# Kernel optimization log

Hardware: AMD Instinct MI355X
Metric: run time of the kernel (lower is better)

Reference implementation:

```python
import jax, jax.numpy as jnp
import numpy as np
import math

HIDDEN = 2048
NUM_HEADS = 32
NUM_KV_HEADS = 8
HEAD_DIM = HIDDEN // NUM_HEADS  # 64
GROUPS = NUM_HEADS // NUM_KV_HEADS  # 4
ROPE_THETA = 10000.0
TOPK_FRAC = 0.5
BSZ, QLEN = 1, 2048


def setup_inputs() -> dict:
    key = jax.random.key(0)
    ks = jax.random.split(key, 6)
    s = 0.02
    return {
        "hidden_states": jax.random.normal(ks[0], (BSZ, QLEN, HIDDEN), jnp.float32),
        "Wq": jax.random.normal(ks[1], (HIDDEN, HIDDEN), jnp.float32) * s,
        "Wk": jax.random.normal(ks[2], (NUM_KV_HEADS * HEAD_DIM, HIDDEN), jnp.float32) * s,
        "Wv": jax.random.normal(ks[3], (NUM_KV_HEADS * HEAD_DIM, HIDDEN), jnp.float32) * s,
        "Wo": jax.random.normal(ks[4], (HIDDEN, HIDDEN), jnp.float32) * s,
        "Wpred": jax.random.normal(ks[5], (NUM_HEADS, HIDDEN), jnp.float32) * s,
        "position_ids": jnp.tile(jnp.arange(QLEN, dtype=jnp.int32), (BSZ, 1)),
    }


def _rotate_half(x):
    h = x.shape[-1] // 2
    return jnp.concatenate([-x[..., h:], x[..., :h]], axis=-1)


def _rope_cos_sin(position_ids, dtype):
    inv_freq = 1.0 / (ROPE_THETA ** (jnp.arange(0, HEAD_DIM, 2, dtype=jnp.float32) / HEAD_DIM))
    freqs = position_ids.astype(jnp.float32)[..., None] * inv_freq  # [b, q, d/2]
    emb = jnp.concatenate([freqs, freqs], axis=-1)                  # [b, q, d]
    return jnp.cos(emb).astype(dtype), jnp.sin(emb).astype(dtype)


def _head_mask(hidden_states, Wpred):
    # predictor logits per token -> top-k heads -> binary mask [b, H, q]
    logits = jnp.einsum('bqh,nh->bqn', hidden_states.astype(jnp.float32), Wpred.astype(jnp.float32))
    k = int(NUM_HEADS * TOPK_FRAC)
    _, idx = jax.lax.top_k(logits, k)                    # [b, q, k]
    mask = jax.nn.one_hot(idx, NUM_HEADS, dtype=hidden_states.dtype).sum(axis=-2)  # [b, q, H]
    return jax.lax.stop_gradient(jnp.swapaxes(mask, 1, 2))  # [b, H, q]


def reference(hidden_states, Wq, Wk, Wv, Wo, Wpred, position_ids):
    b, q_len, _ = hidden_states.shape
    dtype = hidden_states.dtype

    head_mask = _head_mask(hidden_states, Wpred)

    q = (hidden_states @ Wq.T).reshape(b, q_len, NUM_HEADS, HEAD_DIM).transpose(0, 2, 1, 3)
    k = (hidden_states @ Wk.T).reshape(b, q_len, NUM_KV_HEADS, HEAD_DIM).transpose(0, 2, 1, 3)
    v = (hidden_states @ Wv.T).reshape(b, q_len, NUM_KV_HEADS, HEAD_DIM).transpose(0, 2, 1, 3)

    cos, sin = _rope_cos_sin(position_ids, dtype)  # [b, q, d]
    cos, sin = cos[:, None], sin[:, None]          # [b, 1, q, d]
    q = q * cos + _rotate_half(q) * sin
    k = k * cos + _rotate_half(k) * sin

    # repeat_kv (GQA)
    k = jnp.repeat(k, GROUPS, axis=1)  # [b, H, q, d]
    v = jnp.repeat(v, GROUPS, axis=1)

    scores = jnp.einsum('bhqd,bhkd->bhqk', q, k) / math.sqrt(HEAD_DIM)
    causal = jnp.triu(jnp.full((q_len, q_len), -1e9, dtype=scores.dtype), k=1)
    scores = scores + causal
    attn = jax.nn.softmax(scores.astype(jnp.float32), axis=-1).astype(dtype)

    out = jnp.einsum('bhqk,bhkd->bhqd', attn, v)
    out = out * head_mask[..., None]               # gate inactive heads
    out = out.transpose(0, 2, 1, 3).reshape(b, q_len, HIDDEN)
    return out @ Wo.T
```

## Files before the change

### kernel.cpp

```cpp
#include <hip/hip_runtime.h>
#include <hip/hip_bf16.h>

#define HIDDEN 2048
#define NHEADS 32
#define NKV 8
#define HD 64
#define QLEN 2048

typedef short bf16x8 __attribute__((ext_vector_type(8)));
typedef float f32x4 __attribute__((ext_vector_type(4)));
typedef float f32x16 __attribute__((ext_vector_type(16)));

static __device__ __forceinline__ unsigned short f2bf(float f) {
  unsigned int u = __float_as_uint(f);
  u += 0x7fff + ((u >> 16) & 1);
  return (unsigned short)(u >> 16);
}
static __device__ __forceinline__ float bf2f(unsigned short h) {
  return __uint_as_float(((unsigned int)h) << 16);
}
static __device__ __forceinline__ unsigned pack_bf2(float lo, float hi) {
  __hip_bfloat162 h2 = __float22bfloat162_rn(make_float2(lo, hi));
  unsigned u; __builtin_memcpy(&u, &h2, 4); return u;
}

#define GL16(gsrc, ldst) \
  __builtin_amdgcn_global_load_lds((const __attribute__((address_space(1))) unsigned int*)(gsrc), \
                                   (__attribute__((address_space(3))) unsigned int*)(ldst), 16, 0, 0)
#define MFMA32(a, b, c) __builtin_amdgcn_mfma_f32_32x32x16_bf16((a), (b), (c), 0, 0, 0)

__global__ __launch_bounds__(256) void cvt_all_kernel(const float* __restrict__ p0, const float* __restrict__ p1,
                                                      const float* __restrict__ p2, const float* __restrict__ p3,
                                                      const float* __restrict__ p4,
                                                      unsigned short* __restrict__ q0, unsigned short* __restrict__ q1,
                                                      unsigned short* __restrict__ q2, unsigned short* __restrict__ q3,
                                                      unsigned short* __restrict__ q4) {
  const int n0 = 1048576, n1 = 2097152, n2 = 2359296, n3 = 2621440, n4 = 3670016;
  for (int t = blockIdx.x * 256 + threadIdx.x; t < n4; t += gridDim.x * 256) {
    const float4* src; unsigned short* dst; int off;
    if (t < n0)      { src = (const float4*)p0; dst = q0; off = t; }
    else if (t < n1) { src = (const float4*)p1; dst = q1; off = t - n0; }
    else if (t < n2) { src = (const float4*)p2; dst = q2; off = t - n1; }
    else if (t < n3) { src = (const float4*)p3; dst = q3; off = t - n2; }
    else             { src = (const float4*)p4; dst = q4; off = t - n3; }
    float4 v = src[off];
    ushort4 o;
    o.x = f2bf(v.x); o.y = f2bf(v.y); o.z = f2bf(v.z); o.w = f2bf(v.w);
    ((ushort4*)dst)[off] = o;
  }
}

__global__ void rope_table_kernel(const int* __restrict__ pid, float* __restrict__ cost, float* __restrict__ sint) {
  int t = blockIdx.x * blockDim.x + threadIdx.x;
  if (t >= QLEN * 32) return;
  int pos = t >> 5, j = t & 31;
  float p = (float)pid[pos];
  float inv = exp2f(-(float)j * 0.41524101187358740f);
  float f = p * inv;
  cost[t] = cosf(f);
  sint[t] = sinf(f);
}

__global__ __launch_bounds__(256) void wpt_kernel(const float* __restrict__ Wpred, float* __restrict__ WpT) {
  int k = blockIdx.x * 256 + threadIdx.x;
  float v[32];
#pragma unroll
  for (int h = 0; h < 32; ++h) v[h] = Wpred[(size_t)h * HIDDEN + k];
  float4* o = (float4*)(WpT + (size_t)k * 32);
#pragma unroll
  for (int j = 0; j < 8; ++j) o[j] = make_float4(v[4*j], v[4*j+1], v[4*j+2], v[4*j+3]);
}

__global__ __launch_bounds__(256) void headmask_part_kernel(const float* __restrict__ hs,
                                                            const float* __restrict__ WpT,
                                                            double* __restrict__ part) {
  const int tid = threadIdx.x;
  const int ql = tid >> 5, hh = tid & 31;
  const int q = blockIdx.x * 8 + ql;
  const int ks = blockIdx.y;
  const float* hr = hs + (size_t)q * HIDDEN + ks * 512;
  const float* wp = WpT + (size_t)ks * 512 * 32 + hh;
  double a0 = 0.0, a1 = 0.0;
#pragma unroll 4
  for (int k = 0; k < 512; k += 4) {
    float4 hv = *(const float4*)(hr + k);
    float w0 = wp[(k + 0) * 32];
    float w1 = wp[(k + 1) * 32];
    float w2 = wp[(k + 2) * 32];
    float w3 = wp[(k + 3) * 32];
    a0 += (double)hv.x * (double)w0 + (double)hv.y * (double)w1;
    a1 += (double)hv.z * (double)w2 + (double)hv.w * (double)w3;
  }
  part[((size_t)ks * QLEN + q) * 32 + hh] = a0 + a1;
}

__global__ __launch_bounds__(256) void headmask_comb_kernel(const double* __restrict__ part,
                                                            float* __restrict__ mask) {
  __shared__ float lg[8][32];
  const int tid = threadIdx.x;
  const int ql = tid >> 5, hh = tid & 31;
  const int q = blockIdx.x * 8 + ql;
  double s = part[(size_t)q * 32 + hh]
           + part[((size_t)QLEN + q) * 32 + hh]
           + part[((size_t)2 * QLEN + q) * 32 + hh]
           + part[((size_t)3 * QLEN + q) * 32 + hh];
  float mine = (float)s;
  lg[ql][hh] = mine;
  __syncthreads();
  int rank = 0;
#pragma unroll
  for (int j = 0; j < NHEADS; ++j) {
    float oj = lg[ql][j];
    if (oj > mine || (oj == mine && j < hh)) ++rank;
  }
  mask[(size_t)hh * QLEN + q] = (rank < 16) ? 1.0f : 0.0f;
}

__global__ void rope_apply_kernel(unsigned short* __restrict__ X,
                                  const float* __restrict__ cost, const float* __restrict__ sint,
                                  int nh, int rowstride, int total) {
  int t = blockIdx.x * blockDim.x + threadIdx.x;
  if (t >= total) return;
  int j = t & 31;
  int h = (t >> 5) % nh;
  int pos = t / (32 * nh);
  size_t base = (size_t)pos * rowstride + h * HD;
  float x0 = bf2f(X[base + j]);
  float x1 = bf2f(X[base + 32 + j]);
  float c = cost[pos * 32 + j];
  float s = sint[pos * 32 + j];
  X[base + j]      = f2bf(x0 * c - x1 * s);
  X[base + 32 + j] = f2bf(x1 * c + x0 * s);
}

__global__ __launch_bounds__(256) void transpose_kernel(const unsigned short* __restrict__ in,
                                                        unsigned short* __restrict__ out,
                                                        int R, int C, int ldin) {
  __shared__ unsigned short t[64][72];
  int r0 = blockIdx.y * 64, c0 = blockIdx.x * 64;
  int tid = threadIdx.x;
  int rr = tid >> 3;
  int cc = (tid & 7) * 8;
#pragma unroll
  for (int c = 0; c < 2; ++c) {
    int row = rr + c * 32;
    *(bf16x8*)&t[row][cc] = *(const bf16x8*)(in + (size_t)(r0 + row) * ldin + c0 + cc);
  }
  __syncthreads();
#pragma unroll
  for (int c = 0; c < 2; ++c) {
    int oc = rr + c * 32;
    union { unsigned short s[8]; bf16x8 v; } o;
#pragma unroll
    for (int j = 0; j < 8; ++j) o.s[j] = t[cc + j][oc];
    *(bf16x8*)(out + (size_t)(c0 + oc) * R + r0 + cc) = o.v;
  }
}

template<bool OUT_BF16>
__global__ __launch_bounds__(256) void gemm2_kernel(const unsigned short* __restrict__ A,
                                                    const unsigned short* __restrict__ B,
                                                    void* __restrict__ Cout, int N, int K) {
  __shared__ __align__(16) unsigned short As[128 * 32];
  __shared__ __align__(16) unsigned short Bs[128 * 32];
  const int tid = threadIdx.x;
  const int w = tid >> 6, l = tid & 63;
  const int lr = l & 15, lg = l >> 4;
  const int n0 = blockIdx.x * 128, m0 = blockIdx.y * 128;
  const int wm = (w >> 1) * 64, wn = (w & 1) * 64;
  f32x4 acc[4][4] = {};
  const int srow = w * 16 + (l >> 2);
  const int scol = (l & 3) * 8;
  const unsigned short* ap0 = A + (size_t)(m0 + srow) * K + scol;
  const unsigned short* ap1 = ap0 + (size_t)64 * K;
  const unsigned short* bp0 = B + (size_t)(n0 + srow) * K + scol;
  const unsigned short* bp1 = bp0 + (size_t)64 * K;
  unsigned short* asl0 = As + w * 512;
  unsigned short* asl1 = As + 2048 + w * 512;
  unsigned short* bsl0 = Bs + w * 512;
  unsigned short* bsl1 = Bs + 2048 + w * 512;
  for (int k0 = 0; k0 < K; k0 += 32) {
    GL16(ap0 + k0, asl0);
    GL16(ap1 + k0, asl1);
    GL16(bp0 + k0, bsl0);
    GL16(bp1 + k0, bsl1);
    __syncthreads();
    bf16x8 af[4], bfr[4];
#pragma unroll
    for (int m = 0; m < 4; ++m) af[m] = *(const bf16x8*)(As + (wm + m * 16 + lr) * 32 + lg * 8);
#pragma unroll
    for (int n = 0; n < 4; ++n) bfr[n] = *(const bf16x8*)(Bs + (wn + n * 16 + lr) * 32 + lg * 8);
#pragma unroll
    for (int m = 0; m < 4; ++m)
#pragma unroll
      for (int n = 0; n < 4; ++n)
        acc[m][n] = __builtin_amdgcn_mfma_f32_16x16x32_bf16(af[m], bfr[n], acc[m][n], 0, 0, 0);
    __syncthreads();
  }
#pragma unroll
  for (int m = 0; m < 4; ++m) {
    int row = m0 + wm + m * 16 + lg * 4;
#pragma unroll
    for (int n = 0; n < 4; ++n) {
      int col = n0 + wn + n * 16 + lr;
#pragma unroll
      for (int r = 0; r < 4; ++r) {
        if (OUT_BF16)
          ((unsigned short*)Cout)[(size_t)(row + r) * N + col] = f2bf(acc[m][n][r]);
        else
          ((float*)Cout)[(size_t)(row + r) * N + col] = acc[m][n][r];
      }
    }
  }
}

__global__ __launch_bounds__(128) void attn5_kernel(const unsigned short* __restrict__ Q,
                                                    const unsigned short* __restrict__ KV,
                                                    const unsigned short* __restrict__ VT,
                                                    const float* __restrict__ cost,
                                                    const float* __restrict__ sint,
                                                    const float* __restrict__ mask,
                                                    unsigned short* __restrict__ AO) {
  __shared__ __align__(16) unsigned short sm[2][4096];
  const int tid = threadIdx.x;
  const int w = tid >> 6, l = tid & 63;
  const int hi = l >> 5, l31 = l & 31;
  const int h = blockIdx.y, kvh = h >> 2;
  const int qt = 31 - blockIdx.x;
  const int qrow = qt * 64 + w * 32 + l31;
  const int swz = (l & 7) << 4;
  const int hi16 = hi << 4;
  const float DEFER_T = 11.5415603f;

  const int strow = l >> 3;
  const int scol = ((l & 7) ^ strow) * 8;
  const unsigned short* kp0 = KV + (size_t)((0 + w) * 8 + strow) * 1024 + kvh * 64 + scol;
  const unsigned short* kp1 = KV + (size_t)((2 + w) * 8 + strow) * 1024 + kvh * 64 + scol;
  const unsigned short* kp2 = KV + (size_t)((4 + w) * 8 + strow) * 1024 + kvh * 64 + scol;
  const unsigned short* kp3 = KV + (size_t)((6 + w) * 8 + strow) * 1024 + kvh * 64 + scol;

#define STAGE(kt_, b_) do { \
    const size_t kko_ = (size_t)(kt_) * 65536; \
    unsigned short* smb_ = &sm[b_][0]; \
    GL16(kp0 + kko_, smb_ + (0 + w) * 512); \
    GL16(kp1 + kko_, smb_ + (2 + w) * 512); \
    GL16(kp2 + kko_, smb_ + (4 + w) * 512); \
    GL16(kp3 + kko_, smb_ + (6 + w) * 512); \
  } while (0)

  const float QSC = 0.125f * 1.44269504088896340736f;
  const unsigned short* qp = Q + (size_t)qrow * HIDDEN + h * HD + hi * 8;
  bf16x8 qv0 = *(const bf16x8*)qp;
  bf16x8 qv1 = *(const bf16x8*)(qp + 16);
  bf16x8 qv2 = *(const bf16x8*)(qp + 32);
  bf16x8 qv3 = *(const bf16x8*)(qp + 48);
  const float* cbp = cost + qrow * 32 + hi * 8;
  const float* sbp = sint + qrow * 32 + hi * 8;
  f32x4 ca0 = *(const f32x4*)cbp,        ca1 = *(const f32x4*)(cbp + 4);
  f32x4 cB0 = *(const f32x4*)(cbp + 16), cB1 = *(const f32x4*)(cbp + 20);
  f32x4 sa0 = *(const f32x4*)sbp,        sa1 = *(const f32x4*)(sbp + 4);
  f32x4 sB0 = *(const f32x4*)(sbp + 16), sB1 = *(const f32x4*)(sbp + 20);
  bf16x8 qr0, qr1, qr2, qr3;
#pragma unroll
  for (int j = 0; j < 8; ++j) {
    float cosA = j < 4 ? ca0[j] : ca1[j - 4];
    float sinA = j < 4 ? sa0[j] : sa1[j - 4];
    float cosB = j < 4 ? cB0[j] : cB1[j - 4];
    float sinB = j < 4 ? sB0[j] : sB1[j - 4];
    float x0 = bf2f((unsigned short)qv0[j]);
    float x1 = bf2f((unsigned short)qv1[j]);
    float x2 = bf2f((unsigned short)qv2[j]);
    float x3 = bf2f((unsigned short)qv3[j]);
    qr0[j] = (short)f2bf((x0 * cosA - x2 * sinA) * QSC);
    qr1[j] = (short)f2bf((x1 * cosB - x3 * sinB) * QSC);
    qr2[j] = (short)f2bf((x2 * cosA + x0 * sinA) * QSC);
    qr3[j] = (short)f2bf((x3 * cosB + x1 * sinB) * QSC);
  }

  f32x16 O0 = {}, O1 = {};
  float mR = -1e30f, sR = 0.f;
  int cur = 0;
  STAGE(0, 0);
  __syncthreads();

  for (int kt = 0; kt <= qt; ++kt) {
    if (kt < qt) STAGE(kt + 1, cur ^ 1);

    const char* Kc = (const char*)&sm[cur][0];

    f32x16 sA = {}, sB = {};
#define KF(half, dc) (*(const bf16x8*)(Kc + (((half) * 32 + l31) << 7) + ((((dc) * 32 + hi16)) ^ swz)))
    sA = MFMA32(KF(0, 0), qr0, sA);
    sA = MFMA32(KF(0, 1), qr1, sA);
    sA = MFMA32(KF(0, 2), qr2, sA);
    sA = MFMA32(KF(0, 3), qr3, sA);
    sB = MFMA32(KF(1, 0), qr0, sB);
    sB = MFMA32(KF(1, 1), qr1, sB);
    sB = MFMA32(KF(1, 2), qr2, sB);
    sB = MFMA32(KF(1, 3), qr3, sB);
#undef KF

    bf16x8 vf[2][4];
#pragma unroll
    for (int n = 0; n < 2; ++n)
#pragma unroll
      for (int kc = 0; kc < 4; ++kc)
        vf[n][kc] = *(const bf16x8*)(VT + (size_t)(kvh * 64 + n * 32 + l31) * QLEN
                                        + kt * 64 + kc * 16 + hi * 8);

    if (kt == qt) {
      const int wql = w * 32 + l31;
#pragma unroll
      for (int r = 0; r < 16; ++r) {
        int key = (r & 3) + 8 * (r >> 2) + 4 * hi;
        if (key > wql) sA[r] = -1e30f;
        if (32 + key > wql) sB[r] = -1e30f;
      }
    }

#define MAX8(v, o) fmaxf(fmaxf(fmaxf(v[o], v[o+1]), fmaxf(v[o+2], v[o+3])), \
                         fmaxf(fmaxf(v[o+4], v[o+5]), fmaxf(v[o+6], v[o+7])))
    float mx = fmaxf(fmaxf(MAX8(sA, 0), MAX8(sA, 8)), fmaxf(MAX8(sB, 0), MAX8(sB, 8)));
#undef MAX8
    mx = fmaxf(mx, __shfl_xor(mx, 32));
    bool renorm = __any(mx - mR > DEFER_T);
    if (renorm) {
      float mn = fmaxf(mR, mx);
      float sc = exp2f(mR - mn);
      mR = mn;
      sR *= sc;
#pragma unroll
      for (int r = 0; r < 16; ++r) { O0[r] *= sc; O1[r] *= sc; }
    }
#pragma unroll
    for (int r = 0; r < 16; ++r) sA[r] = exp2f(sA[r] - mR);
#pragma unroll
    for (int r = 0; r < 16; ++r) sB[r] = exp2f(sB[r] - mR);
#define SUM8(v, o) (((v[o] + v[o+1]) + (v[o+2] + v[o+3])) + ((v[o+4] + v[o+5]) + (v[o+6] + v[o+7])))
    float rs = (SUM8(sA, 0) + SUM8(sA, 8)) + (SUM8(sB, 0) + SUM8(sB, 8));
#undef SUM8
    rs += __shfl_xor(rs, 32);
    sR += rs;

    bf16x8 pf[4];
#pragma unroll
    for (int kc = 0; kc < 4; ++kc) {
      const int r0 = (kc & 1) * 8;
      float p0, p1, p2, p3, p4, p5, p6, p7;
      if (kc & 2) { p0 = sB[r0+0]; p1 = sB[r0+1]; p2 = sB[r0+2]; p3 = sB[r0+3];
                    p4 = sB[r0+4]; p5 = sB[r0+5]; p6 = sB[r0+6]; p7 = sB[r0+7]; }
      else        { p0 = sA[r0+0]; p1 = sA[r0+1]; p2 = sA[r0+2]; p3 = sA[r0+3];
                    p4 = sA[r0+4]; p5 = sA[r0+5]; p6 = sA[r0+6]; p7 = sA[r0+7]; }
      unsigned a_ = pack_bf2(p0, p1);
      unsigned c_ = pack_bf2(p2, p3);
      unsigned b_ = pack_bf2(p4, p5);
      unsigned d_ = pack_bf2(p6, p7);
      unsigned ax = __shfl_xor(a_, 32), bx2 = __shfl_xor(b_, 32);
      unsigned cx = __shfl_xor(c_, 32), dx = __shfl_xor(d_, 32);
      union { unsigned u[4]; bf16x8 v; } uu;
      uu.u[0] = hi ? bx2 : a_;
      uu.u[1] = hi ? dx : c_;
      uu.u[2] = hi ? b_ : ax;
      uu.u[3] = hi ? d_ : cx;
      pf[kc] = uu.v;
    }

    O0 = MFMA32(vf[0][0], pf[0], O0);
    O1 = MFMA32(vf[1][0], pf[0], O1);
    O0 = MFMA32(vf[0][1], pf[1], O0);
    O1 = MFMA32(vf[1][1], pf[1], O1);
    O0 = MFMA32(vf[0][2], pf[2], O0);
    O1 = MFMA32(vf[1][2], pf[2], O1);
    O0 = MFMA32(vf[0][3], pf[3], O0);
    O1 = MFMA32(vf[1][3], pf[3], O1);

    __syncthreads();
    cur ^= 1;
  }

  float msk = mask[(size_t)h * QLEN + qrow];
  float inv = msk / sR;
  unsigned short* aop = AO + (size_t)qrow * HIDDEN + h * HD;
#pragma unroll
  for (int rp = 0; rp < 8; ++rp) {
    int r = rp * 2;
    int d0 = (r & 3) + 8 * (r >> 2) + 4 * hi;
    *(unsigned*)(aop + d0)      = pack_bf2(O0[r] * inv, O0[r + 1] * inv);
    *(unsigned*)(aop + 32 + d0) = pack_bf2(O1[r] * inv, O1[r + 1] * inv);
  }
#undef STAGE
}

extern "C" void kernel_launch(void* const* d_in, const int* in_sizes, int n_in,
                              void* d_out, int out_size, void* d_ws, size_t ws_size,
                              hipStream_t stream) {
  const float* hs    = (const float*)d_in[0];
  const float* Wq    = (const float*)d_in[1];
  const float* Wk    = (const float*)d_in[2];
  const float* Wv    = (const float*)d_in[3];
  const float* Wo    = (const float*)d_in[4];
  const float* Wpred = (const float*)d_in[5];
  const int*   pid   = (const int*)d_in[6];
  float* out = (float*)d_out;

  unsigned short* hsb = (unsigned short*)d_ws;
  unsigned short* Wqb = hsb + 4194304;
  unsigned short* Wkb = Wqb + 4194304;
  unsigned short* Wvb = Wkb + 1048576;
  unsigned short* Wob = Wvb + 1048576;
  unsigned short* Qb  = Wob + 4194304;
  unsigned short* KVb = Qb  + 4194304;
  unsigned short* AOb = KVb + 2097152;
  float* maskb = (float*)(AOb + 4194304);
  float* cost  = maskb + 65536;
  float* sint  = cost + 65536;
  float* WpT   = sint + 65536;
  double* hmp  = (double*)(WpT + 65536);
  unsigned short* VTb = hsb;

  cvt_all_kernel<<<2048, 256, 0, stream>>>(hs, Wq, Wk, Wv, Wo, hsb, Wqb, Wkb, Wvb, Wob);

  rope_table_kernel<<<256, 256, 0, stream>>>(pid, cost, sint);

  wpt_kernel<<<8, 256, 0, stream>>>(Wpred, WpT);
  headmask_part_kernel<<<dim3(256, 4), 256, 0, stream>>>(hs, WpT, hmp);
  headmask_comb_kernel<<<256, 256, 0, stream>>>(hmp, maskb);

  gemm2_kernel<true><<<dim3(16, 16), 256, 0, stream>>>(hsb, Wqb, Qb, 2048, 2048);
  gemm2_kernel<true><<<dim3(8, 16), 256, 0, stream>>>(hsb, Wkb, KVb, 1024, 2048);

  rope_apply_kernel<<<2048, 256, 0, stream>>>(KVb, cost, sint, NKV, 1024, QLEN * NKV * 32);

  transpose_kernel<<<dim3(8, 32), 256, 0, stream>>>(KVb + 512, VTb, QLEN, 512, 1024);

  attn5_kernel<<<dim3(32, 32), 128, 0, stream>>>(Qb, KVb, VTb, cost, sint, maskb, AOb);

  gemm2_kernel<false><<<dim3(16, 16), 256, 0, stream>>>(AOb, Wob, out, 2048, 2048);
}
```

Baseline: 374.8 us.

## Fuse Q and KV projections into one GEMM; widen attention tile and stage V in LDS

The Q and KV projection GEMMs merge into one launch over a 24-column grid, which relies on Wq, Wk and Wv sitting contiguously in memory as one combined weight. The attention kernel now handles 128 query rows per block with 4 waves, so each K/V tile staged into LDS is shared by twice as many queries. V tiles are also staged into LDS alongside K instead of being read from global memory per wave. Waves whose causal range ends early skip compute but still join the barriers, which adds some idle time and halves the block count.

```diff
diff --git a/kernel.cpp b/kernel.cpp
--- a/kernel.cpp
+++ b/kernel.cpp
@@ -154,6 +154,64 @@
 #pragma unroll
     for (int j = 0; j < 8; ++j) o.s[j] = t[cc + j][oc];
     *(bf16x8*)(out + (size_t)(c0 + oc) * R + r0 + cc) = o.v;
+  }
+}
+
+__global__ __launch_bounds__(256) void gemm_qkv_kernel(const unsigned short* __restrict__ A,
+                                                       const unsigned short* __restrict__ B,
+                                                       unsigned short* __restrict__ Qo,
+                                                       unsigned short* __restrict__ KVo) {
+  const int K = 2048;
+  __shared__ __align__(16) unsigned short As[128 * 32];
+  __shared__ __align__(16) unsigned short Bs[128 * 32];
+  const int tid = threadIdx.x;
+  const int w = tid >> 6, l = tid & 63;
+  const int lr = l & 15, lg = l >> 4;
+  const int n0 = blockIdx.x * 128, m0 = blockIdx.y * 128;
+  const int wm = (w >> 1) * 64, wn = (w & 1) * 64;
+  f32x4 acc[4][4] = {};
+  const int srow = w * 16 + (l >> 2);
+  const int scol = (l & 3) * 8;
+  const unsigned short* ap0 = A + (size_t)(m0 + srow) * K + scol;
+  const unsigned short* ap1 = ap0 + (size_t)64 * K;
+  const unsigned short* bp0 = B + (size_t)(n0 + srow) * K + scol;
+  const unsigned short* bp1 = bp0 + (size_t)64 * K;
+  unsigned short* asl0 = As + w * 512;
+  unsigned short* asl1 = As + 2048 + w * 512;
+  unsigned short* bsl0 = Bs + w * 512;
+  unsigned short* bsl1 = Bs + 2048 + w * 512;
+  for (int k0 = 0; k0 < K; k0 += 32) {
+    GL16(ap0 + k0, asl0);
+    GL16(ap1 + k0, asl1);
+    GL16(bp0 + k0, bsl0);
+    GL16(bp1 + k0, bsl1);
+    __syncthreads();
+    bf16x8 af[4], bfr[4];
+#pragma unroll
+    for (int m = 0; m < 4; ++m) af[m] = *(const bf16x8*)(As + (wm + m * 16 + lr) * 32 + lg * 8);
+#pragma unroll
+    for (int n = 0; n < 4; ++n) bfr[n] = *(const bf16x8*)(Bs + (wn + n * 16 + lr) * 32 + lg * 8);
+#pragma unroll
+    for (int m = 0; m < 4; ++m)
+#pragma unroll
+      for (int n = 0; n < 4; ++n)
+        acc[m][n] = __builtin_amdgcn_mfma_f32_16x16x32_bf16(af[m], bfr[n], acc[m][n], 0, 0, 0);
+    __syncthreads();
+  }
+  unsigned short* Cp;
+  int ldc, cb;
+  if (n0 < 2048) { Cp = Qo;  ldc = 2048; cb = n0; }
+  else           { Cp = KVo; ldc = 1024; cb = n0 - 2048; }
+#pragma unroll
+  for (int m = 0; m < 4; ++m) {
+    int row = m0 + wm + m * 16 + lg * 4;
+#pragma unroll
+    for (int n = 0; n < 4; ++n) {
+      int col = cb + wn + n * 16 + lr;
+#pragma unroll
+      for (int r = 0; r < 4; ++r)
+        Cp[(size_t)(row + r) * ldc + col] = f2bf(acc[m][n][r]);
+    }
   }
 }
 
@@ -214,38 +272,39 @@
   }
 }
 
-__global__ __launch_bounds__(128) void attn5_kernel(const unsigned short* __restrict__ Q,
+__global__ __launch_bounds__(256) void attn6_kernel(const unsigned short* __restrict__ Q,
                                                     const unsigned short* __restrict__ KV,
                                                     const unsigned short* __restrict__ VT,
                                                     const float* __restrict__ cost,
                                                     const float* __restrict__ sint,
                                                     const float* __restrict__ mask,
                                                     unsigned short* __restrict__ AO) {
-  __shared__ __align__(16) unsigned short sm[2][4096];
+  __shared__ __align__(16) unsigned short sm[2][8192];
   const int tid = threadIdx.x;
   const int w = tid >> 6, l = tid & 63;
   const int hi = l >> 5, l31 = l & 31;
   const int h = blockIdx.y, kvh = h >> 2;
-  const int qt = 31 - blockIdx.x;
-  const int qrow = qt * 64 + w * 32 + l31;
+  const int qt = 15 - blockIdx.x;
+  const int qrow = qt * 128 + w * 32 + l31;
   const int swz = (l & 7) << 4;
   const int hi16 = hi << 4;
   const float DEFER_T = 11.5415603f;
+  const int nt = 2 * qt + 2;
+  const int dt = 2 * qt + (w >> 1);
 
   const int strow = l >> 3;
-  const int scol = ((l & 7) ^ strow) * 8;
-  const unsigned short* kp0 = KV + (size_t)((0 + w) * 8 + strow) * 1024 + kvh * 64 + scol;
-  const unsigned short* kp1 = KV + (size_t)((2 + w) * 8 + strow) * 1024 + kvh * 64 + scol;
-  const unsigned short* kp2 = KV + (size_t)((4 + w) * 8 + strow) * 1024 + kvh * 64 + scol;
-  const unsigned short* kp3 = KV + (size_t)((6 + w) * 8 + strow) * 1024 + kvh * 64 + scol;
+  const int scol = ((l & 7) ^ (strow & 7)) * 8;
+  const unsigned short* kpA = KV + (size_t)(w * 8 + strow) * 1024 + kvh * 64 + scol;
+  const unsigned short* kpB = kpA + (size_t)32 * 1024;
+  const unsigned short* vpA = VT + (size_t)(kvh * 64 + w * 8 + strow) * QLEN + scol;
+  const unsigned short* vpB = vpA + (size_t)32 * QLEN;
 
 #define STAGE(kt_, b_) do { \
-    const size_t kko_ = (size_t)(kt_) * 65536; \
     unsigned short* smb_ = &sm[b_][0]; \
-    GL16(kp0 + kko_, smb_ + (0 + w) * 512); \
-    GL16(kp1 + kko_, smb_ + (2 + w) * 512); \
-    GL16(kp2 + kko_, smb_ + (4 + w) * 512); \
-    GL16(kp3 + kko_, smb_ + (6 + w) * 512); \
+    GL16(kpA + (size_t)(kt_) * 65536, smb_ + w * 512); \
+    GL16(kpB + (size_t)(kt_) * 65536, smb_ + 2048 + w * 512); \
+    GL16(vpA + (size_t)(kt_) * 64,    smb_ + 4096 + w * 512); \
+    GL16(vpB + (size_t)(kt_) * 64,    smb_ + 6144 + w * 512); \
   } while (0)
 
   const float QSC = 0.125f * 1.44269504088896340736f;
@@ -283,96 +342,92 @@
   STAGE(0, 0);
   __syncthreads();
 
-  for (int kt = 0; kt <= qt; ++kt) {
-    if (kt < qt) STAGE(kt + 1, cur ^ 1);
-
-    const char* Kc = (const char*)&sm[cur][0];
-
-    f32x16 sA = {}, sB = {};
+  for (int kt = 0; kt < nt; ++kt) {
+    if (kt + 1 < nt) STAGE(kt + 1, cur ^ 1);
+
+    if (kt <= dt) {
+      const char* Kc = (const char*)&sm[cur][0];
+      const char* Vc = Kc + 8192;
+
+      f32x16 sA = {}, sB = {};
 #define KF(half, dc) (*(const bf16x8*)(Kc + (((half) * 32 + l31) << 7) + ((((dc) * 32 + hi16)) ^ swz)))
-    sA = MFMA32(KF(0, 0), qr0, sA);
-    sA = MFMA32(KF(0, 1), qr1, sA);
-    sA = MFMA32(KF(0, 2), qr2, sA);
-    sA = MFMA32(KF(0, 3), qr3, sA);
-    sB = MFMA32(KF(1, 0), qr0, sB);
-    sB = MFMA32(KF(1, 1), qr1, sB);
-    sB = MFMA32(KF(1, 2), qr2, sB);
-    sB = MFMA32(KF(1, 3), qr3, sB);
+      sA = MFMA32(KF(0, 0), qr0, sA);
+      sA = MFMA32(KF(0, 1), qr1, sA);
+      sA = MFMA32(KF(0, 2), qr2, sA);
+      sA = MFMA32(KF(0, 3), qr3, sA);
+      sB = MFMA32(KF(1, 0), qr0, sB);
+      sB = MFMA32(KF(1, 1), qr1, sB);
+      sB = MFMA32(KF(1, 2), qr2, sB);
+      sB = MFMA32(KF(1, 3), qr3, sB);
 #undef KF
 
-    bf16x8 vf[2][4];
-#pragma unroll
-    for (int n = 0; n < 2; ++n)
-#pragma unroll
-      for (int kc = 0; kc < 4; ++kc)
-        vf[n][kc] = *(const bf16x8*)(VT + (size_t)(kvh * 64 + n * 32 + l31) * QLEN
-                                        + kt * 64 + kc * 16 + hi * 8);
-
-    if (kt == qt) {
-      const int wql = w * 32 + l31;
-#pragma unroll
-      for (int r = 0; r < 16; ++r) {
-        int key = (r & 3) + 8 * (r >> 2) + 4 * hi;
-        if (key > wql) sA[r] = -1e30f;
-        if (32 + key > wql) sB[r] = -1e30f;
+      if (kt == dt) {
+#pragma unroll
+        for (int r = 0; r < 16; ++r) {
+          int key = kt * 64 + (r & 3) + 8 * (r >> 2) + 4 * hi;
+          if (key > qrow) sA[r] = -1e30f;
+          if (key + 32 > qrow) sB[r] = -1e30f;
+        }
       }
-    }
 
 #define MAX8(v, o) fmaxf(fmaxf(fmaxf(v[o], v[o+1]), fmaxf(v[o+2], v[o+3])), \
                          fmaxf(fmaxf(v[o+4], v[o+5]), fmaxf(v[o+6], v[o+7])))
-    float mx = fmaxf(fmaxf(MAX8(sA, 0), MAX8(sA, 8)), fmaxf(MAX8(sB, 0), MAX8(sB, 8)));
+      float mx = fmaxf(fmaxf(MAX8(sA, 0), MAX8(sA, 8)), fmaxf(MAX8(sB, 0), MAX8(sB, 8)));
 #undef MAX8
-    mx = fmaxf(mx, __shfl_xor(mx, 32));
-    bool renorm = __any(mx - mR > DEFER_T);
-    if (renorm) {
-      float mn = fmaxf(mR, mx);
-      float sc = exp2f(mR - mn);
-      mR = mn;
-      sR *= sc;
-#pragma unroll
-      for (int r = 0; r < 16; ++r) { O0[r] *= sc; O1[r] *= sc; }
+      mx = fmaxf(mx, __shfl_xor(mx, 32));
+      bool renorm = __any(mx - mR > DEFER_T);
+      if (renorm) {
+        float mn = fmaxf(mR, mx);
+        float sc = exp2f(mR - mn);
+        mR = mn;
+        sR *= sc;
+#pragma unroll
+        for (int r = 0; r < 16; ++r) { O0[r] *= sc; O1[r] *= sc; }
+      }
+#pragma unroll
+      for (int r = 0; r < 16; ++r) sA[r] = exp2f(sA[r] - mR);
+#pragma unroll
+      for (int r = 0; r < 16; ++r) sB[r] = exp2f(sB[r] - mR);
+#define SUM8(v, o) (((v[o] + v[o+1]) + (v[o+2] + v[o+3])) + ((v[o+4] + v[o+5]) + (v[o+6] + v[o+7])))
+      float rs = (SUM8(sA, 0) + SUM8(sA, 8)) + (SUM8(sB, 0) + SUM8(sB, 8));
+#undef SUM8
+      rs += __shfl_xor(rs, 32);
+      sR += rs;
+
+      bf16x8 pf[4];
+#pragma unroll
+      for (int kc = 0; kc < 4; ++kc) {
+        const int r0 = (kc & 1) * 8;
+        float p0, p1, p2, p3, p4, p5, p6, p7;
+        if (kc & 2) { p0 = sB[r0+0]; p1 = sB[r0+1]; p2 = sB[r0+2]; p3 = sB[r0+3];
+                      p4 = sB[r0+4]; p5 = sB[r0+5]; p6 = sB[r0+6]; p7 = sB[r0+7]; }
+        else        { p0 = sA[r0+0]; p1 = sA[r0+1]; p2 = sA[r0+2]; p3 = sA[r0+3];
+                      p4 = sA[r0+4]; p5 = sA[r0+5]; p6 = sA[r0+6]; p7 = sA[r0+7]; }
+        unsigned a_ = pack_bf2(p0, p1);
+        unsigned c_ = pack_bf2(p2, p3);
+        unsigned b_ = pack_bf2(p4, p5);
+        unsigned d_ = pack_bf2(p6, p7);
+        unsigned ax = __shfl_xor(a_, 32), bx2 = __shfl_xor(b_, 32);
+        unsigned cx = __shfl_xor(c_, 32), dx = __shfl_xor(d_, 32);
+        union { unsigned u[4]; bf16x8 v; } uu;
+        uu.u[0] = hi ? bx2 : a_;
+        uu.u[1] = hi ? dx : c_;
+        uu.u[2] = hi ? b_ : ax;
+        uu.u[3] = hi ? d_ : cx;
+        pf[kc] = uu.v;
+      }
+
+#define VF(n, kc) (*(const bf16x8*)(Vc + (((n) * 32 + l31) << 7) + ((((kc) * 32 + hi16)) ^ swz)))
+      O0 = MFMA32(VF(0, 0), pf[0], O0);
+      O1 = MFMA32(VF(1, 0), pf[0], O1);
+      O0 = MFMA32(VF(0, 1), pf[1], O0);
+      O1 = MFMA32(VF(1, 1), pf[1], O1);
+      O0 = MFMA32(VF(0, 2), pf[2], O0);
+      O1 = MFMA32(VF(1, 2), pf[2], O1);
+      O0 = MFMA32(VF(0, 3), pf[3], O0);
+      O1 = MFMA32(VF(1, 3), pf[3], O1);
+#undef VF
     }
-#pragma unroll
-    for (int r = 0; r < 16; ++r) sA[r] = exp2f(sA[r] - mR);
-#pragma unroll
-    for (int r = 0; r < 16; ++r) sB[r] = exp2f(sB[r] - mR);
-#define SUM8(v, o) (((v[o] + v[o+1]) + (v[o+2] + v[o+3])) + ((v[o+4] + v[o+5]) + (v[o+6] + v[o+7])))
-    float rs = (SUM8(sA, 0) + SUM8(sA, 8)) + (SUM8(sB, 0) + SUM8(sB, 8));
-#undef SUM8
-    rs += __shfl_xor(rs, 32);
-    sR += rs;
-
-    bf16x8 pf[4];
-#pragma unroll
-    for (int kc = 0; kc < 4; ++kc) {
-      const int r0 = (kc & 1) * 8;
-      float p0, p1, p2, p3, p4, p5, p6, p7;
-      if (kc & 2) { p0 = sB[r0+0]; p1 = sB[r0+1]; p2 = sB[r0+2]; p3 = sB[r0+3];
-                    p4 = sB[r0+4]; p5 = sB[r0+5]; p6 = sB[r0+6]; p7 = sB[r0+7]; }
-      else        { p0 = sA[r0+0]; p1 = sA[r0+1]; p2 = sA[r0+2]; p3 = sA[r0+3];
-                    p4 = sA[r0+4]; p5 = sA[r0+5]; p6 = sA[r0+6]; p7 = sA[r0+7]; }
-      unsigned a_ = pack_bf2(p0, p1);
-      unsigned c_ = pack_bf2(p2, p3);
-      unsigned b_ = pack_bf2(p4, p5);
-      unsigned d_ = pack_bf2(p6, p7);
-      unsigned ax = __shfl_xor(a_, 32), bx2 = __shfl_xor(b_, 32);
-      unsigned cx = __shfl_xor(c_, 32), dx = __shfl_xor(d_, 32);
-      union { unsigned u[4]; bf16x8 v; } uu;
-      uu.u[0] = hi ? bx2 : a_;
-      uu.u[1] = hi ? dx : c_;
-      uu.u[2] = hi ? b_ : ax;
-      uu.u[3] = hi ? d_ : cx;
-      pf[kc] = uu.v;
-    }
-
-    O0 = MFMA32(vf[0][0], pf[0], O0);
-    O1 = MFMA32(vf[1][0], pf[0], O1);
-    O0 = MFMA32(vf[0][1], pf[1], O0);
-    O1 = MFMA32(vf[1][1], pf[1], O1);
-    O0 = MFMA32(vf[0][2], pf[2], O0);
-    O1 = MFMA32(vf[1][2], pf[2], O1);
-    O0 = MFMA32(vf[0][3], pf[3], O0);
-    O1 = MFMA32(vf[1][3], pf[3], O1);
 
     __syncthreads();
     cur ^= 1;
@@ -426,14 +481,13 @@
   headmask_part_kernel<<<dim3(256, 4), 256, 0, stream>>>(hs, WpT, hmp);
   headmask_comb_kernel<<<256, 256, 0, stream>>>(hmp, maskb);
 
-  gemm2_kernel<true><<<dim3(16, 16), 256, 0, stream>>>(hsb, Wqb, Qb, 2048, 2048);
-  gemm2_kernel<true><<<dim3(8, 16), 256, 0, stream>>>(hsb, Wkb, KVb, 1024, 2048);
+  gemm_qkv_kernel<<<dim3(24, 16), 256, 0, stream>>>(hsb, Wqb, Qb, KVb);
 
   rope_apply_kernel<<<2048, 256, 0, stream>>>(KVb, cost, sint, NKV, 1024, QLEN * NKV * 32);
 
   transpose_kernel<<<dim3(8, 32), 256, 0, stream>>>(KVb + 512, VTb, QLEN, 512, 1024);
 
-  attn5_kernel<<<dim3(32, 32), 128, 0, stream>>>(Qb, KVb, VTb, cost, sint, maskb, AOb);
+  attn6_kernel<<<dim3(16, 32), 256, 0, stream>>>(Qb, KVb, VTb, cost, sint, maskb, AOb);
 
   gemm2_kernel<false><<<dim3(16, 16), 256, 0, stream>>>(AOb, Wob, out, 2048, 2048);
 }
```

Measured after the change: 327.9 us. -12.5%, faster.
